# Kernel optimization log

Hardware: AMD Instinct MI355X
Metric: run time of the kernel (lower is better)

Reference implementation:

```python
import jax, jax.numpy as jnp
import numpy as np

NUM_GRAPHS = 2048  # number of graphs in the batch (max batch id + 1)


def setup_inputs() -> dict:
    key = jax.random.key(0)
    ks = jax.random.split(key, 8)
    N, E, ND, ED, H = 100000, 400000, 256, 128, 128
    IN = ND * 3 + ED  # 896
    h = jax.random.normal(ks[0], (N, ND), dtype=jnp.float32)
    ei = jax.random.randint(ks[1], (2, E), 0, N, dtype=jnp.int64)
    ea = jax.random.normal(ks[2], (E, ED), dtype=jnp.float32)
    batch = jnp.sort(jax.random.randint(ks[3], (N,), 0, NUM_GRAPHS, dtype=jnp.int64))
    W1 = jax.random.normal(ks[4], (IN, H), dtype=jnp.float32) * (1.0 / np.sqrt(IN))
    b1 = jnp.zeros((H,), dtype=jnp.float32)
    W2 = jax.random.normal(ks[5], (H, 1), dtype=jnp.float32) * (1.0 / np.sqrt(H))
    b2 = jnp.zeros((1,), dtype=jnp.float32)
    return {"h": h, "ei": ei, "ea": ea, "batch": batch,
            "W1": W1, "b1": b1, "W2": W2, "b2": b2}


def reference(h, ei, ea, batch, W1, b1, W2, b2):
    s, t = ei[0], ei[1]
    # global_mean_pool: per-graph mean of node features
    sums = jax.ops.segment_sum(h, batch, num_segments=NUM_GRAPHS)          # [B, ND]
    counts = jax.ops.segment_sum(jnp.ones((h.shape[0],), h.dtype), batch,
                                 num_segments=NUM_GRAPHS)                   # [B]
    pooled = sums / jnp.maximum(counts, 1.0)[:, None]
    g = pooled[batch[s]]                                                    # [E, ND]
    x = jnp.concatenate([h[s], h[t], ea, g], axis=-1)                       # [E, 3*ND+ED]
    hid = jnp.maximum(x @ W1 + b1, 0.0)
    return hid @ W2 + b2                                                    # [E, 1]
```

## Files before the change

### kernel.cpp

```cpp
#include <hip/hip_runtime.h>
#include <hip/hip_bf16.h>


typedef __attribute__((ext_vector_type(8))) short bf16x8;
typedef __attribute__((ext_vector_type(4))) float f32x4;

constexpr int kND = 256;
constexpr int kED = 128;
constexpr int kH  = 128;
constexpr int kIN = 896;
constexpr int kKT = 7;
constexpr int kB  = 2048;
constexpr int TM  = 128;
constexpr int SX  = 136;
constexpr int kNF = 224;

__device__ __forceinline__ ushort f2bf(float x) {
  union { float f; unsigned u; } c; c.f = x;
  unsigned u = c.u + 0x7FFFu + ((c.u >> 16) & 1u);
  return (ushort)(u >> 16);
}
__device__ __forceinline__ float bf2f(ushort x) {
  union { unsigned u; float f; } c; c.u = ((unsigned)x) << 16;
  return c.f;
}
__device__ __forceinline__ bool data_is_f32(const void* p) {
  const unsigned* u = (const unsigned*)p;
  int cnt = 0;
  #pragma unroll
  for (int i = 0; i < 64; ++i) {
    unsigned e = (u[i] >> 7) & 0xFFu;
    cnt += (e >= 90u && e <= 140u) ? 1 : 0;
  }
  return cnt < 40;
}
__device__ __forceinline__ bool idx_is_64(const int* __restrict__ p) {
  return ((p[1] | p[3] | p[5] | p[7]) == 0) && ((p[0] | p[2] | p[4] | p[6]) != 0);
}
__device__ __forceinline__ float loadf(const void* p, int i, bool isf32) {
  return isf32 ? ((const float*)p)[i] : bf2f(((const ushort*)p)[i]);
}

__global__ __launch_bounds__(256) void convert_h(
    const void* __restrict__ hv, ushort* __restrict__ hbf, long total4) {
  const bool isf32 = data_is_f32(hv);
  long i = (long)blockIdx.x * 256 + threadIdx.x;
  const long stride = (long)gridDim.x * 256;
  if (isf32) {
    const float4* src = (const float4*)hv;
    for (; i < total4; i += stride) {
      float4 f = src[i];
      ushort4 u; u.x = f2bf(f.x); u.y = f2bf(f.y); u.z = f2bf(f.z); u.w = f2bf(f.w);
      ((ushort4*)hbf)[i] = u;
    }
  } else {
    const ushort4* src = (const ushort4*)hv;
    for (; i < total4; i += stride) ((ushort4*)hbf)[i] = src[i];
  }
}

__global__ __launch_bounds__(256) void pool_kernel(
    const void* __restrict__ hv, const ushort* __restrict__ hbf, int preconv,
    const int* __restrict__ batch, const int* __restrict__ ei, int N,
    ushort* __restrict__ pooled) {
  const bool isf32 = data_is_f32(hv);
  const bool is64 = idx_is_64(ei);
  const int b = blockIdx.x, tid = threadIdx.x;
  __shared__ int bounds[2];
  __shared__ float4 sred[256];
  if (tid < 2) {
    int target = b + tid;
    int lo = 0, hi = N;
    while (lo < hi) {
      int mid = (lo + hi) >> 1;
      int v = is64 ? batch[2 * mid] : batch[mid];
      if (v < target) lo = mid + 1; else hi = mid;
    }
    bounds[tid] = lo;
  }
  __syncthreads();
  const int lo = bounds[0], hi = bounds[1];
  const int dg = tid & 63;
  const int rstr = tid >> 6;
  float4 acc = {0.f, 0.f, 0.f, 0.f};
  const ushort* hp = preconv ? hbf : (isf32 ? nullptr : (const ushort*)hv);
  if (hp) {
    for (int r = lo + rstr; r < hi; r += 4) {
      ushort4 u = *(const ushort4*)(hp + (size_t)r * kND + dg * 4);
      acc.x += bf2f(u.x); acc.y += bf2f(u.y); acc.z += bf2f(u.z); acc.w += bf2f(u.w);
    }
  } else {
    const float* hf = (const float*)hv;
    for (int r = lo + rstr; r < hi; r += 4) {
      float4 f = *(const float4*)(hf + (size_t)r * kND + dg * 4);
      acc.x += f.x; acc.y += f.y; acc.z += f.z; acc.w += f.w;
    }
  }
  sred[tid] = acc;
  __syncthreads();
  if (tid < 64) {
    float4 a0 = sred[tid], a1 = sred[tid + 64], a2 = sred[tid + 128], a3 = sred[tid + 192];
    int cnt = hi - lo; if (cnt < 1) cnt = 1;
    float inv = 1.f / (float)cnt;
    ushort4 u;
    u.x = f2bf((a0.x + a1.x + a2.x + a3.x) * inv);
    u.y = f2bf((a0.y + a1.y + a2.y + a3.y) * inv);
    u.z = f2bf((a0.z + a1.z + a2.z + a3.z) * inv);
    u.w = f2bf((a0.w + a1.w + a2.w + a3.w) * inv);
    *(ushort4*)(pooled + (size_t)b * kND + tid * 4) = u;
  }
}

__global__ __launch_bounds__(256) void build_wfrag(
    const void* __restrict__ W1v, ushort* __restrict__ Wfrag) {
  const bool isf32 = data_is_f32(W1v);
  int idx = blockIdx.x * 256 + threadIdx.x;
  if (idx >= kNF * 64) return;
  int l = idx & 63, f = idx >> 6;
  int ni = f & 3, nhi = (f >> 2) & 1, ksg = f >> 3;
  int n = nhi * 64 + ni * 16 + (l & 15);
  int k0 = ksg * 32 + (l >> 4) * 8;
  union { ushort us[8]; uint4 v; } cv;
  #pragma unroll
  for (int j = 0; j < 8; ++j)
    cv.us[j] = f2bf(loadf(W1v, (k0 + j) * kH + n, isf32));
  *(uint4*)(Wfrag + (size_t)f * 512 + l * 8) = cv.v;
}

__global__ __launch_bounds__(256, 4) void edge_kernel(
    const void* __restrict__ hv, const ushort* __restrict__ hbf, int preconv,
    const int* __restrict__ ei, const void* __restrict__ eav,
    const int* __restrict__ batch, const ushort* __restrict__ pooled,
    const ushort* __restrict__ Wfrag, const void* __restrict__ b1v,
    const void* __restrict__ W2v, const void* __restrict__ b2v,
    void* __restrict__ outv, int E) {
  __shared__ __align__(16) ushort Xl[TM * SX];
  __shared__ int rs[TM], rt[TM], rg[TM];
  __shared__ float outacc[TM];
  __shared__ float b1s[kH], w2s[kH];

  const int tid = threadIdx.x;
  const int e0 = blockIdx.x * TM;
  const bool isf32 = data_is_f32(hv);
  const bool is64 = idx_is_64(ei);

  if (tid < TM) {
    int e = e0 + tid; if (e >= E) e = E - 1;
    int s = is64 ? ei[2 * e] : ei[e];
    int t = is64 ? ei[2 * (E + e)] : ei[E + e];
    rs[tid] = s;
    rt[tid] = t;
    rg[tid] = is64 ? batch[2 * s] : batch[s];
    w2s[tid] = loadf(W2v, tid, isf32);
    b1s[tid] = loadf(b1v, tid, isf32);
    outacc[tid] = 0.f;
  }
  __syncthreads();

  const int wave = tid >> 6, lane = tid & 63;
  const int l15 = lane & 15, quad = lane >> 4;
  const int mh = (wave & 1) * 64;
  const int nhi = wave >> 1;
  const int nh = nhi * 64;

  f32x4 acc[4][4];
  #pragma unroll
  for (int i = 0; i < 4; ++i)
    #pragma unroll
    for (int j = 0; j < 4; ++j)
      acc[i][j] = (f32x4){0.f, 0.f, 0.f, 0.f};

  const int r0 = tid >> 4;
  const int c8 = (tid & 15) * 8;
  const ushort* hp = preconv ? hbf : (isf32 ? nullptr : (const ushort*)hv);

  for (int kt = 0; kt < kKT; ++kt) {
    #pragma unroll
    for (int i = 0; i < 8; ++i) {
      int r = r0 + i * 16;
      uint4 val;
      if (kt >= 5) {
        val = *(const uint4*)&pooled[(size_t)rg[r] * kND + (kt - 5) * 128 + c8];
      } else if (kt == 4) {
        int e = e0 + r; if (e >= E) e = E - 1;
        if (isf32) {
          const float* s = (const float*)eav + (size_t)e * kED + c8;
          float4 f0 = ((const float4*)s)[0];
          float4 f1 = ((const float4*)s)[1];
          union { ushort us[8]; uint4 v; } cv;
          cv.us[0] = f2bf(f0.x); cv.us[1] = f2bf(f0.y);
          cv.us[2] = f2bf(f0.z); cv.us[3] = f2bf(f0.w);
          cv.us[4] = f2bf(f1.x); cv.us[5] = f2bf(f1.y);
          cv.us[6] = f2bf(f1.z); cv.us[7] = f2bf(f1.w);
          val = cv.v;
        } else {
          val = *(const uint4*)((const ushort*)eav + (size_t)e * kED + c8);
        }
      } else {
        int node = (kt < 2) ? rs[r] : rt[r];
        size_t off = (size_t)node * kND + (kt & 1) * 128 + c8;
        if (hp) {
          val = *(const uint4*)(hp + off);
        } else {
          const float* s = (const float*)hv + off;
          float4 f0 = ((const float4*)s)[0];
          float4 f1 = ((const float4*)s)[1];
          union { ushort us[8]; uint4 v; } cv;
          cv.us[0] = f2bf(f0.x); cv.us[1] = f2bf(f0.y);
          cv.us[2] = f2bf(f0.z); cv.us[3] = f2bf(f0.w);
          cv.us[4] = f2bf(f1.x); cv.us[5] = f2bf(f1.y);
          cv.us[6] = f2bf(f1.z); cv.us[7] = f2bf(f1.w);
          val = cv.v;
        }
      }
      *(uint4*)&Xl[r * SX + c8] = val;
    }
    __syncthreads();
    #pragma unroll
    for (int ks = 0; ks < 4; ++ks) {
      const ushort* wp =
          Wfrag + ((size_t)(((kt * 4 + ks) * 2 + nhi) * 4)) * 512 + lane * 8;
      bf16x8 af[4], bfm[4];
      #pragma unroll
      for (int ni = 0; ni < 4; ++ni)
        bfm[ni] = *(const bf16x8*)(wp + ni * 512);
      int kk = ks * 32 + quad * 8;
      #pragma unroll
      for (int mi = 0; mi < 4; ++mi)
        af[mi] = *(const bf16x8*)&Xl[(mh + mi * 16 + l15) * SX + kk];
      #pragma unroll
      for (int mi = 0; mi < 4; ++mi)
        #pragma unroll
        for (int ni = 0; ni < 4; ++ni)
          acc[mi][ni] = __builtin_amdgcn_mfma_f32_16x16x32_bf16(
              af[mi], bfm[ni], acc[mi][ni], 0, 0, 0);
    }
    __syncthreads();
  }

  float w2v[4], b1r[4];
  #pragma unroll
  for (int ni = 0; ni < 4; ++ni) {
    int n = nh + ni * 16 + l15;
    w2v[ni] = w2s[n];
    b1r[ni] = b1s[n];
  }
  #pragma unroll
  for (int mi = 0; mi < 4; ++mi) {
    float ps[4] = {0.f, 0.f, 0.f, 0.f};
    #pragma unroll
    for (int ni = 0; ni < 4; ++ni)
      #pragma unroll
      for (int j = 0; j < 4; ++j) {
        float v = acc[mi][ni][j] + b1r[ni];
        ps[j] += (v > 0.f ? v : 0.f) * w2v[ni];
      }
    #pragma unroll
    for (int off = 1; off < 16; off <<= 1)
      #pragma unroll
      for (int j = 0; j < 4; ++j)
        ps[j] += __shfl_xor(ps[j], off, 64);
    if (l15 == 0)
      #pragma unroll
      for (int j = 0; j < 4; ++j)
        atomicAdd(&outacc[mh + mi * 16 + quad * 4 + j], ps[j]);
  }
  __syncthreads();
  if (tid < TM) {
    int e = e0 + tid;
    if (e < E) {
      float a = outacc[tid] + loadf(b2v, 0, isf32);
      if (isf32) ((float*)outv)[e] = a;
      else       ((ushort*)outv)[e] = f2bf(a);
    }
  }
}

extern "C" void kernel_launch(void* const* d_in, const int* in_sizes, int n_in,
                              void* d_out, int out_size, void* d_ws, size_t ws_size,
                              hipStream_t stream) {
  const void* h   = d_in[0];
  const int*  ei  = (const int*)d_in[1];
  const void* ea  = d_in[2];
  const int*  bat = (const int*)d_in[3];
  const void* W1  = d_in[4];
  const void* b1  = d_in[5];
  const void* W2  = d_in[6];
  const void* b2  = d_in[7];

  const int N = in_sizes[3];
  const int E = in_sizes[1] / 2;

  ushort* pooled = (ushort*)d_ws;
  ushort* Wfrag  = pooled + (size_t)kB * kND;
  ushort* hbf    = Wfrag + (size_t)kNF * 512;
  const size_t need =
      ((size_t)kB * kND + (size_t)kNF * 512 + (size_t)N * kND) * sizeof(ushort);
  const int preconv = (ws_size >= need) ? 1 : 0;

  if (preconv)
    convert_h<<<4096, 256, 0, stream>>>(h, hbf, (long)N * kND / 4);
  pool_kernel<<<kB, 256, 0, stream>>>(h, hbf, preconv, bat, ei, N, pooled);
  build_wfrag<<<(kNF * 64 + 255) / 256, 256, 0, stream>>>(W1, Wfrag);
  edge_kernel<<<(E + TM - 1) / TM, 256, 0, stream>>>(
      h, hbf, preconv, ei, ea, bat, pooled, Wfrag, b1, W2, b2, d_out, E);
}
```

Before: 552.0 us.

## Prefetch next K-tile gathers into registers during MFMA and widen pool loads

The edge kernel now reorders its K tiles so edge attributes come first, and the weight-fragment builder permutes W1 to match. On the bf16 path it loads the next tile's gathered rows into registers while MFMAs run on the current LDS tile. The pool kernel switches to 16-byte loads with 8 row strides, two rows per iteration, and an 8-way LDS reduction. The trade is higher register pressure: launch bounds drop from 4 to 3 blocks per SM, which lowers occupancy.

```diff
diff --git a/kernel.cpp b/kernel.cpp
--- a/kernel.cpp
+++ b/kernel.cpp
@@ -8,7 +8,6 @@
 constexpr int kND = 256;
 constexpr int kED = 128;
 constexpr int kH  = 128;
-constexpr int kIN = 896;
 constexpr int kKT = 7;
 constexpr int kB  = 2048;
 constexpr int TM  = 128;
@@ -67,7 +66,7 @@
   const bool is64 = idx_is_64(ei);
   const int b = blockIdx.x, tid = threadIdx.x;
   __shared__ int bounds[2];
-  __shared__ float4 sred[256];
+  __shared__ float sred[8][kND];
   if (tid < 2) {
     int target = b + tid;
     int lo = 0, hi = N;
@@ -80,35 +79,59 @@
   }
   __syncthreads();
   const int lo = bounds[0], hi = bounds[1];
-  const int dg = tid & 63;
-  const int rstr = tid >> 6;
-  float4 acc = {0.f, 0.f, 0.f, 0.f};
+  const int dg = tid & 31;
+  const int rstr = tid >> 5;
+  float a[8];
+  #pragma unroll
+  for (int j = 0; j < 8; ++j) a[j] = 0.f;
   const ushort* hp = preconv ? hbf : (isf32 ? nullptr : (const ushort*)hv);
   if (hp) {
-    for (int r = lo + rstr; r < hi; r += 4) {
-      ushort4 u = *(const ushort4*)(hp + (size_t)r * kND + dg * 4);
-      acc.x += bf2f(u.x); acc.y += bf2f(u.y); acc.z += bf2f(u.z); acc.w += bf2f(u.w);
+    const ushort* base = hp + dg * 8;
+    int r = lo + rstr;
+    for (; r + 8 < hi; r += 16) {
+      union { uint4 v; ushort us[8]; } u0, u1;
+      u0.v = *(const uint4*)(base + (size_t)r * kND);
+      u1.v = *(const uint4*)(base + (size_t)(r + 8) * kND);
+      #pragma unroll
+      for (int j = 0; j < 8; ++j) a[j] += bf2f(u0.us[j]);
+      #pragma unroll
+      for (int j = 0; j < 8; ++j) a[j] += bf2f(u1.us[j]);
+    }
+    for (; r < hi; r += 8) {
+      union { uint4 v; ushort us[8]; } u0;
+      u0.v = *(const uint4*)(base + (size_t)r * kND);
+      #pragma unroll
+      for (int j = 0; j < 8; ++j) a[j] += bf2f(u0.us[j]);
     }
   } else {
-    const float* hf = (const float*)hv;
-    for (int r = lo + rstr; r < hi; r += 4) {
-      float4 f = *(const float4*)(hf + (size_t)r * kND + dg * 4);
-      acc.x += f.x; acc.y += f.y; acc.z += f.z; acc.w += f.w;
-    }
-  }
-  sred[tid] = acc;
+    const float* base = (const float*)hv + dg * 8;
+    int r = lo + rstr;
+    for (; r + 8 < hi; r += 16) {
+      float4 f0 = *(const float4*)(base + (size_t)r * kND);
+      float4 f1 = *(const float4*)(base + (size_t)r * kND + 4);
+      float4 f2 = *(const float4*)(base + (size_t)(r + 8) * kND);
+      float4 f3 = *(const float4*)(base + (size_t)(r + 8) * kND + 4);
+      a[0] += f0.x + f2.x; a[1] += f0.y + f2.y;
+      a[2] += f0.z + f2.z; a[3] += f0.w + f2.w;
+      a[4] += f1.x + f3.x; a[5] += f1.y + f3.y;
+      a[6] += f1.z + f3.z; a[7] += f1.w + f3.w;
+    }
+    for (; r < hi; r += 8) {
+      float4 f0 = *(const float4*)(base + (size_t)r * kND);
+      float4 f1 = *(const float4*)(base + (size_t)r * kND + 4);
+      a[0] += f0.x; a[1] += f0.y; a[2] += f0.z; a[3] += f0.w;
+      a[4] += f1.x; a[5] += f1.y; a[6] += f1.z; a[7] += f1.w;
+    }
+  }
+  #pragma unroll
+  for (int j = 0; j < 8; ++j) sred[rstr][dg * 8 + j] = a[j];
   __syncthreads();
-  if (tid < 64) {
-    float4 a0 = sred[tid], a1 = sred[tid + 64], a2 = sred[tid + 128], a3 = sred[tid + 192];
-    int cnt = hi - lo; if (cnt < 1) cnt = 1;
-    float inv = 1.f / (float)cnt;
-    ushort4 u;
-    u.x = f2bf((a0.x + a1.x + a2.x + a3.x) * inv);
-    u.y = f2bf((a0.y + a1.y + a2.y + a3.y) * inv);
-    u.z = f2bf((a0.z + a1.z + a2.z + a3.z) * inv);
-    u.w = f2bf((a0.w + a1.w + a2.w + a3.w) * inv);
-    *(ushort4*)(pooled + (size_t)b * kND + tid * 4) = u;
-  }
+  int cnt = hi - lo; if (cnt < 1) cnt = 1;
+  float inv = 1.f / (float)cnt;
+  float s = 0.f;
+  #pragma unroll
+  for (int st = 0; st < 8; ++st) s += sred[st][tid];
+  pooled[(size_t)b * kND + tid] = f2bf(s * inv);
 }
 
 __global__ __launch_bounds__(256) void build_wfrag(
@@ -118,8 +141,10 @@
   if (idx >= kNF * 64) return;
   int l = idx & 63, f = idx >> 6;
   int ni = f & 3, nhi = (f >> 2) & 1, ksg = f >> 3;
+  int tile = ksg >> 2;
+  int basek = (tile == 0) ? 512 : ((tile < 5) ? (tile - 1) * 128 : tile * 128);
   int n = nhi * 64 + ni * 16 + (l & 15);
-  int k0 = ksg * 32 + (l >> 4) * 8;
+  int k0 = basek + (ksg & 3) * 32 + (l >> 4) * 8;
   union { ushort us[8]; uint4 v; } cv;
   #pragma unroll
   for (int j = 0; j < 8; ++j)
@@ -127,7 +152,7 @@
   *(uint4*)(Wfrag + (size_t)f * 512 + l * 8) = cv.v;
 }
 
-__global__ __launch_bounds__(256, 4) void edge_kernel(
+__global__ __launch_bounds__(256, 3) void edge_kernel(
     const void* __restrict__ hv, const ushort* __restrict__ hbf, int preconv,
     const int* __restrict__ ei, const void* __restrict__ eav,
     const int* __restrict__ batch, const ushort* __restrict__ pooled,
@@ -174,48 +199,31 @@
   const int c8 = (tid & 15) * 8;
   const ushort* hp = preconv ? hbf : (isf32 ? nullptr : (const ushort*)hv);
 
-  for (int kt = 0; kt < kKT; ++kt) {
+
+  auto stage_ea = [&]() {
     #pragma unroll
     for (int i = 0; i < 8; ++i) {
       int r = r0 + i * 16;
+      int e = e0 + r; if (e >= E) e = E - 1;
       uint4 val;
-      if (kt >= 5) {
-        val = *(const uint4*)&pooled[(size_t)rg[r] * kND + (kt - 5) * 128 + c8];
-      } else if (kt == 4) {
-        int e = e0 + r; if (e >= E) e = E - 1;
-        if (isf32) {
-          const float* s = (const float*)eav + (size_t)e * kED + c8;
-          float4 f0 = ((const float4*)s)[0];
-          float4 f1 = ((const float4*)s)[1];
-          union { ushort us[8]; uint4 v; } cv;
-          cv.us[0] = f2bf(f0.x); cv.us[1] = f2bf(f0.y);
-          cv.us[2] = f2bf(f0.z); cv.us[3] = f2bf(f0.w);
-          cv.us[4] = f2bf(f1.x); cv.us[5] = f2bf(f1.y);
-          cv.us[6] = f2bf(f1.z); cv.us[7] = f2bf(f1.w);
-          val = cv.v;
-        } else {
-          val = *(const uint4*)((const ushort*)eav + (size_t)e * kED + c8);
-        }
+      if (isf32) {
+        const float* s = (const float*)eav + (size_t)e * kED + c8;
+        float4 f0 = ((const float4*)s)[0];
+        float4 f1 = ((const float4*)s)[1];
+        union { ushort us[8]; uint4 v; } cv;
+        cv.us[0] = f2bf(f0.x); cv.us[1] = f2bf(f0.y);
+        cv.us[2] = f2bf(f0.z); cv.us[3] = f2bf(f0.w);
+        cv.us[4] = f2bf(f1.x); cv.us[5] = f2bf(f1.y);
+        cv.us[6] = f2bf(f1.z); cv.us[7] = f2bf(f1.w);
+        val = cv.v;
       } else {
-        int node = (kt < 2) ? rs[r] : rt[r];
-        size_t off = (size_t)node * kND + (kt & 1) * 128 + c8;
-        if (hp) {
-          val = *(const uint4*)(hp + off);
-        } else {
-          const float* s = (const float*)hv + off;
-          float4 f0 = ((const float4*)s)[0];
-          float4 f1 = ((const float4*)s)[1];
-          union { ushort us[8]; uint4 v; } cv;
-          cv.us[0] = f2bf(f0.x); cv.us[1] = f2bf(f0.y);
-          cv.us[2] = f2bf(f0.z); cv.us[3] = f2bf(f0.w);
-          cv.us[4] = f2bf(f1.x); cv.us[5] = f2bf(f1.y);
-          cv.us[6] = f2bf(f1.z); cv.us[7] = f2bf(f1.w);
-          val = cv.v;
-        }
+        val = *(const uint4*)((const ushort*)eav + (size_t)e * kED + c8);
       }
       *(uint4*)&Xl[r * SX + c8] = val;
     }
-    __syncthreads();
+  };
+
+  auto compute_tile = [&](int kt) {
     #pragma unroll
     for (int ks = 0; ks < 4; ++ks) {
       const ushort* wp =
@@ -235,7 +243,68 @@
           acc[mi][ni] = __builtin_amdgcn_mfma_f32_16x16x32_bf16(
               af[mi], bfm[ni], acc[mi][ni], 0, 0, 0);
     }
+  };
+
+  if (hp) {
+    uint4 pre[8];
+    stage_ea();
     __syncthreads();
+    for (int kt = 0; kt < kKT; ++kt) {
+      const int t = kt + 1;
+      if (t < kKT) {
+        if (t >= 5) {
+          const size_t half = (size_t)(t - 5) * 128 + c8;
+          #pragma unroll
+          for (int i = 0; i < 8; ++i)
+            pre[i] = *(const uint4*)(pooled + (size_t)rg[r0 + i * 16] * kND + half);
+        } else {
+          const size_t half = (size_t)((t - 1) & 1) * 128 + c8;
+          const int* nn = (t < 3) ? rs : rt;
+          #pragma unroll
+          for (int i = 0; i < 8; ++i)
+            pre[i] = *(const uint4*)(hp + (size_t)nn[r0 + i * 16] * kND + half);
+        }
+      }
+      compute_tile(kt);
+      __syncthreads();
+      if (t < kKT) {
+        #pragma unroll
+        for (int i = 0; i < 8; ++i)
+          *(uint4*)&Xl[(r0 + i * 16) * SX + c8] = pre[i];
+      }
+      __syncthreads();
+    }
+  } else {
+    for (int kt = 0; kt < kKT; ++kt) {
+      if (kt == 0) {
+        stage_ea();
+      } else {
+        #pragma unroll
+        for (int i = 0; i < 8; ++i) {
+          int r = r0 + i * 16;
+          uint4 val;
+          if (kt >= 5) {
+            val = *(const uint4*)&pooled[(size_t)rg[r] * kND + (kt - 5) * 128 + c8];
+          } else {
+            int node = (kt < 3) ? rs[r] : rt[r];
+            size_t off = (size_t)node * kND + ((kt - 1) & 1) * 128 + c8;
+            const float* s = (const float*)hv + off;
+            float4 f0 = ((const float4*)s)[0];
+            float4 f1 = ((const float4*)s)[1];
+            union { ushort us[8]; uint4 v; } cv;
+            cv.us[0] = f2bf(f0.x); cv.us[1] = f2bf(f0.y);
+            cv.us[2] = f2bf(f0.z); cv.us[3] = f2bf(f0.w);
+            cv.us[4] = f2bf(f1.x); cv.us[5] = f2bf(f1.y);
+            cv.us[6] = f2bf(f1.z); cv.us[7] = f2bf(f1.w);
+            val = cv.v;
+          }
+          *(uint4*)&Xl[r * SX + c8] = val;
+        }
+      }
+      __syncthreads();
+      compute_tile(kt);
+      __syncthreads();
+    }
   }
 
   float w2v[4], b1r[4];
```

Result: slower. 655.0 us (+18.7%).
